# Optimization experiments

Measured on AMD Instinct MI355X. Metric: run time of the kernel, lower is better.

Reference implementation:

```python
import jax, jax.numpy as jnp
import numpy as np

N_NODES = 50000
IN_FEAT = 500
HIDDEN = 128
K = 2
N_CLASS = 16
E1 = 1000000
E2 = 1500000


def setup_inputs() -> dict:
    key = jax.random.key(0)
    ks = jax.random.split(key, 9)
    x = jax.random.normal(ks[0], (N_NODES, IN_FEAT), dtype=jnp.float32)
    a1_rows = jax.random.randint(ks[1], (E1,), 0, N_NODES, dtype=jnp.int32)
    a1_cols = jax.random.randint(ks[2], (E1,), 0, N_NODES, dtype=jnp.int32)
    a1_vals = jax.random.uniform(ks[3], (E1,), dtype=jnp.float32)
    a2_rows = jax.random.randint(ks[4], (E2,), 0, N_NODES, dtype=jnp.int32)
    a2_cols = jax.random.randint(ks[5], (E2,), 0, N_NODES, dtype=jnp.int32)
    a2_vals = jax.random.uniform(ks[6], (E2,), dtype=jnp.float32)
    w_embed = jax.random.normal(ks[7], (IN_FEAT, HIDDEN), dtype=jnp.float32) * 0.05
    w_classify = jax.random.normal(ks[8], ((2 ** (K + 1) - 1) * HIDDEN, N_CLASS), dtype=jnp.float32) * 0.05
    return {"x": x, "a1_rows": a1_rows, "a1_cols": a1_cols, "a1_vals": a1_vals,
            "a2_rows": a2_rows, "a2_cols": a2_cols, "a2_vals": a2_vals,
            "w_embed": w_embed, "w_classify": w_classify}


def _spmm(rows, cols, vals, r, n):
    # sparse [n,n] (COO) @ dense [n,d] -> gather sources, scale, scatter-add to rows
    return jax.ops.segment_sum(vals[:, None] * r[cols], rows, num_segments=n)


def reference(x, a1_rows, a1_cols, a1_vals, a2_rows, a2_cols, a2_vals, w_embed, w_classify):
    n = x.shape[0]
    rs = [jax.nn.relu(x @ w_embed)]  # [n, hidden]
    for _ in range(K):
        r_last = rs[-1]
        r1 = _spmm(a1_rows, a1_cols, a1_vals, r_last, n)
        r2 = _spmm(a2_rows, a2_cols, a2_vals, r_last, n)
        rs.append(jax.nn.relu(jnp.concatenate([r1, r2], axis=1)))
    r_final = jnp.concatenate(rs, axis=1)  # [n, (2^(k+1)-1)*hidden]
    # dropout is inactive in eval mode
    return jax.nn.softmax(r_final @ w_classify, axis=1)
```

## Files before the change

### kernel.cpp

```cpp
#include <hip/hip_runtime.h>
#include <hip/hip_fp16.h>

#define HID 128
#define INF 500
#define NCLS 16
#define PW  112
#define BKLG 8
#define BKW 256
#define NB1 128
#define NB2 192

typedef __attribute__((ext_vector_type(8))) short short8v;
typedef __attribute__((ext_vector_type(4))) float f32x4;
typedef __attribute__((ext_vector_type(4))) float f4v;

__device__ __forceinline__ void split_bf16(float v, unsigned short& h, unsigned short& l) {
  unsigned u = __float_as_uint(v);
  h = (unsigned short)(u >> 16);
  float hf = __uint_as_float(u & 0xFFFF0000u);
  l = (unsigned short)(__float_as_uint(v - hf) >> 16);
}

__device__ __forceinline__ void cvt8v(f4v c0, f4v c1, short8v& h8, short8v& l8) {
#pragma unroll
  for (int j = 0; j < 8; ++j) {
    float v = (j < 4) ? c0[j] : c1[j - 4];
    unsigned short h, l;
    split_bf16(v, h, l);
    h8[j] = (short)h;
    l8[j] = (short)l;
  }
}

__global__ __launch_bounds__(256) void prep_w(
    const float* __restrict__ we, const float* __restrict__ wc,
    unsigned short* __restrict__ wh, unsigned short* __restrict__ wl,
    unsigned short* __restrict__ ch, unsigned short* __restrict__ cl) {
  const int bid = blockIdx.x;
  if (bid < 256) {
    int idx = bid * 256 + threadIdx.x;
    int k = idx >> 7, nn = idx & 127;
    float v = (k < INF) ? we[k * HID + nn] : 0.f;
    unsigned short h, l;
    split_bf16(v, h, l);
    int kstep = k >> 5, ks = k & 31;
    int lane = (nn & 15) | ((ks >> 3) << 4);
    int j = ks & 7, nf = nn >> 4;
    size_t o = (((size_t)(kstep * 8 + nf)) * 64 + lane) * 8 + j;
    wh[o] = h;
    wl[o] = l;
  } else {
    int idx = (bid - 256) * 256 + threadIdx.x;
    if (idx >= HID * PW) return;
    int k = idx / PW, np = idx % PW;
    int o = np >> 4;
    int blk = (o == 0) ? 0 : ((o < 4) ? (2 * o - 1) : (2 * o - 6));
    float v = wc[(blk * HID + k) * NCLS + (np & 15)];
    unsigned short h, l;
    split_bf16(v, h, l);
    int kstep = k >> 5, ks = k & 31;
    int lane = (np & 15) | ((ks >> 3) << 4);
    int j = ks & 7, nf = np >> 4;
    size_t of = (((size_t)(kstep * 7 + nf)) * 64 + lane) * 8 + j;
    ch[of] = h;
    cl[of] = l;
  }
}

__global__ __launch_bounds__(128) void embed_mfma(
    const float* __restrict__ x, const unsigned short* __restrict__ wh,
    const unsigned short* __restrict__ wl, unsigned short* __restrict__ r0h,
    unsigned short* __restrict__ r0l, int n) {
  const int tid = threadIdx.x;
  const int wave = tid >> 6, lane = tid & 63;
  const int row0 = blockIdx.x * 64;
  const int rA = lane & 15, kg = lane >> 4;

  __shared__ float xs[64][68];

  f32x4 acc[2][8];
#pragma unroll
  for (int rf = 0; rf < 2; ++rf)
#pragma unroll
    for (int nf = 0; nf < 8; ++nf)
#pragma unroll
      for (int r = 0; r < 4; ++r) acc[rf][nf][r] = 0.f;

  f4v pf[8];
#define LOAD_TILE(kt)                                                         \
  {                                                                           \
    const int k0_ = (kt) * 64;                                                \
    _Pragma("unroll")                                                         \
    for (int q = 0; q < 8; ++q) {                                             \
      int i_ = tid + q * 128;                                                 \
      int r_ = i_ >> 4, pos_ = i_ & 15;                                       \
      int gr_ = min(row0 + r_, n - 1);                                        \
      int gk_ = k0_ + pos_ * 4;                                               \
      pf[q] = (gk_ + 4 <= INF)                                                \
                  ? __builtin_nontemporal_load(                               \
                        (const f4v*)&x[(size_t)gr_ * INF + gk_])              \
                  : (f4v)(0.f);                                               \
    }                                                                         \
  }

  LOAD_TILE(0);
  for (int kt = 0; kt < 8; ++kt) {
#pragma unroll
    for (int q = 0; q < 8; ++q) {
      int i = tid + q * 128;
      *(f4v*)&xs[i >> 4][(i & 15) * 4] = pf[q];
    }
    __syncthreads();
    if (kt < 7) LOAD_TILE(kt + 1);

#pragma unroll
    for (int kh2 = 0; kh2 < 2; ++kh2) {
      const int kb = kh2 * 32 + kg * 8;
      short8v ah[2], al[2];
#pragma unroll
      for (int rf = 0; rf < 2; ++rf) {
        const int rl = wave * 32 + rf * 16 + rA;
        f4v c0 = *(const f4v*)&xs[rl][kb];
        f4v c1 = *(const f4v*)&xs[rl][kb + 4];
        cvt8v(c0, c1, ah[rf], al[rf]);
      }
      const size_t bbase = ((size_t)((kt * 2 + kh2) * 8) * 64 + lane) * 8;
      short8v Bh[8], Bl[8];
#pragma unroll
      for (int nf = 0; nf < 8; ++nf) {
        Bh[nf] = *(const short8v*)&wh[bbase + (size_t)nf * 512];
        Bl[nf] = *(const short8v*)&wl[bbase + (size_t)nf * 512];
      }
#pragma unroll
      for (int nf = 0; nf < 8; ++nf)
#pragma unroll
        for (int rf = 0; rf < 2; ++rf) {
          acc[rf][nf] = __builtin_amdgcn_mfma_f32_16x16x32_bf16(ah[rf], Bh[nf], acc[rf][nf], 0, 0, 0);
          acc[rf][nf] = __builtin_amdgcn_mfma_f32_16x16x32_bf16(ah[rf], Bl[nf], acc[rf][nf], 0, 0, 0);
          acc[rf][nf] = __builtin_amdgcn_mfma_f32_16x16x32_bf16(al[rf], Bh[nf], acc[rf][nf], 0, 0, 0);
        }
    }
    __syncthreads();
  }
#undef LOAD_TILE

#pragma unroll
  for (int rf = 0; rf < 2; ++rf)
#pragma unroll
    for (int nf = 0; nf < 8; ++nf) {
      const int row = row0 + wave * 32 + rf * 16 + kg * 4;
      const int col = nf * 16 + rA;
#pragma unroll
      for (int r = 0; r < 4; ++r) {
        if (row + r < n) {
          float v = fmaxf(acc[rf][nf][r], 0.f);
          unsigned short h, l;
          split_bf16(v, h, l);
          r0h[(size_t)(row + r) * HID + col] = h;
          r0l[(size_t)(row + r) * HID + col] = l;
        }
      }
    }
}

__global__ __launch_bounds__(256) void proj_mfma(
    const unsigned short* __restrict__ r0h, const unsigned short* __restrict__ r0l,
    const unsigned short* __restrict__ ch, const unsigned short* __restrict__ cl,
    float* __restrict__ s0f, __half* __restrict__ Pa1, __half* __restrict__ Pa2, int n) {
  const int wave = threadIdx.x >> 6, lane = threadIdx.x & 63;
  const int row0 = blockIdx.x * 64 + wave * 16;
  const int rA = lane & 15, kg = lane >> 4;

  f32x4 acc[7];
#pragma unroll
  for (int nf = 0; nf < 7; ++nf)
#pragma unroll
    for (int r = 0; r < 4; ++r) acc[nf][r] = 0.f;

  const unsigned short* arh = &r0h[(size_t)min(row0 + rA, n - 1) * HID];
  const unsigned short* arl = &r0l[(size_t)min(row0 + rA, n - 1) * HID];

#pragma unroll
  for (int kstep = 0; kstep < 4; ++kstep) {
    const int kb = kstep * 32 + kg * 8;
    short8v ah = __builtin_nontemporal_load((const short8v*)&arh[kb]);
    short8v al = __builtin_nontemporal_load((const short8v*)&arl[kb]);

    const size_t bbase = ((size_t)kstep * 7 * 64 + lane) * 8;
    short8v Bh[7], Bl[7];
#pragma unroll
    for (int nf = 0; nf < 7; ++nf) {
      Bh[nf] = *(const short8v*)&ch[bbase + (size_t)nf * 512];
      Bl[nf] = *(const short8v*)&cl[bbase + (size_t)nf * 512];
    }
#pragma unroll
    for (int nf = 0; nf < 7; ++nf) {
      acc[nf] = __builtin_amdgcn_mfma_f32_16x16x32_bf16(ah, Bh[nf], acc[nf], 0, 0, 0);
      acc[nf] = __builtin_amdgcn_mfma_f32_16x16x32_bf16(ah, Bl[nf], acc[nf], 0, 0, 0);
      acc[nf] = __builtin_amdgcn_mfma_f32_16x16x32_bf16(al, Bh[nf], acc[nf], 0, 0, 0);
    }
  }

#pragma unroll
  for (int nf = 0; nf < 7; ++nf) {
    const int row = row0 + kg * 4;
#pragma unroll
    for (int r = 0; r < 4; ++r) {
      if (row + r < n) {
        float v = acc[nf][r];
        size_t ro = (size_t)(row + r) * 16 + rA;
        if (nf == 0) {
          s0f[ro] = v;
        } else if (nf < 4) {
          Pa1[ro * 4 + (nf - 1)] = __float2half(v);
          if (nf == 1) Pa1[ro * 4 + 3] = __float2half(0.f);
        } else {
          Pa2[ro * 4 + (nf - 4)] = __float2half(v);
          if (nf == 4) Pa2[ro * 4 + 3] = __float2half(0.f);
        }
      }
    }
  }
}

__global__ __launch_bounds__(256) void part_hist(
    const int* __restrict__ r1, int e1, const int* __restrict__ r2, int e2,
    int* __restrict__ g1, int* __restrict__ g2, int nbk) {
  const int m = blockIdx.y;
  const int NB = m ? NB2 : NB1;
  const int b = blockIdx.x;
  if (b >= NB) return;
  const int* rows = m ? r2 : r1;
  const int E = m ? e2 : e1;
  int* g = m ? g2 : g1;
  __shared__ int h[512];
  for (int i = threadIdx.x; i < nbk; i += 256) h[i] = 0;
  __syncthreads();
  const int ch = (E + NB - 1) / NB;
  const int lo = b * ch, hi = min(lo + ch, E);
  for (int i = lo + threadIdx.x; i < hi; i += 256)
    atomicAdd(&h[rows[i] >> BKLG], 1);
  __syncthreads();
  for (int k = threadIdx.x; k < nbk; k += 256) g[(size_t)k * NB + b] = h[k];
}

__global__ __launch_bounds__(256) void part_scan(
    int* __restrict__ g1, int m1, int* __restrict__ g2, int m2) {
  int* g = blockIdx.x ? g2 : g1;
  const int m = blockIdx.x ? m2 : m1;
  __shared__ int sh[256];
  const int t = threadIdx.x;
  const int chunk = (m + 255) >> 8;
  const int lo = t * chunk, hi = min(lo + chunk, m);
  int s = 0;
  for (int i = lo; i < hi; ++i) s += g[i];
  sh[t] = s;
  __syncthreads();
  for (int d = 1; d < 256; d <<= 1) {
    int v = (t >= d) ? sh[t - d] : 0;
    __syncthreads();
    sh[t] += v;
    __syncthreads();
  }
  int run = sh[t] - s;
  for (int i = lo; i < hi; ++i) { int v = g[i]; g[i] = run; run += v; }
}

__global__ __launch_bounds__(256) void part_scatter(
    const int* __restrict__ r1, const int* __restrict__ c1, const float* __restrict__ v1, int e1,
    const int* __restrict__ r2, const int* __restrict__ c2, const float* __restrict__ v2, int e2,
    const int* __restrict__ g1, const int* __restrict__ g2,
    int2* __restrict__ pack1, int2* __restrict__ pack2, int nbk) {
  const int m = blockIdx.y;
  const int NB = m ? NB2 : NB1;
  const int b = blockIdx.x;
  if (b >= NB) return;
  const int* rows = m ? r2 : r1;
  const int* cols = m ? c2 : c1;
  const float* vals = m ? v2 : v1;
  const int E = m ? e2 : e1;
  const int* g = m ? g2 : g1;
  int2* pack = m ? pack2 : pack1;
  __shared__ int lcur[512];
  for (int k = threadIdx.x; k < nbk; k += 256) lcur[k] = g[(size_t)k * NB + b];
  __syncthreads();
  const int ch = (E + NB - 1) / NB;
  const int lo = b * ch, hi = min(lo + ch, E);
  for (int i = lo + threadIdx.x; i < hi; i += 256) {
    int r = rows[i];
    int pos = atomicAdd(&lcur[r >> BKLG], 1);
    unsigned u = (unsigned)(vals[i] * 65536.0f);
    if (u > 65535u) u = 65535u;
    pack[pos] = make_int2(cols[i] | ((r & (BKW - 1)) << 16), (int)u);
  }
}

__global__ __launch_bounds__(256) void bucket_sort(
    const int2* __restrict__ pack1, const int* __restrict__ g1,
    unsigned* __restrict__ srt1, int* __restrict__ rp1, int e1,
    const int2* __restrict__ pack2, const int* __restrict__ g2,
    unsigned* __restrict__ srt2, int* __restrict__ rp2, int e2,
    int n, int nbk) {
  const int m = blockIdx.y;
  const int NB = m ? NB2 : NB1;
  const int2* pack = m ? pack2 : pack1;
  const int* g = m ? g2 : g1;
  unsigned* srt = m ? srt2 : srt1;
  int* rp = m ? rp2 : rp1;
  const int E = m ? e2 : e1;
  const int k = blockIdx.x;
  const int base = g[(size_t)k * NB];
  const int end = (k + 1 < nbk) ? g[(size_t)(k + 1) * NB] : E;
  __shared__ int lcnt[256], lws[256], lcur[256];
  const int t = threadIdx.x;
  lcnt[t] = 0;
  __syncthreads();
  for (int i = base + t; i < end; i += 256)
    atomicAdd(&lcnt[(pack[i].x >> 16) & (BKW - 1)], 1);
  __syncthreads();
  int s = lcnt[t];
  lws[t] = s;
  __syncthreads();
  for (int d = 1; d < 256; d <<= 1) {
    int v = (t >= d) ? lws[t - d] : 0;
    __syncthreads();
    lws[t] += v;
    __syncthreads();
  }
  int excl = base + lws[t] - s;
  lcur[t] = excl;
  int row = k * BKW + t;
  if (row < n) rp[row] = excl;
  if (k == nbk - 1 && t == 0) rp[n] = E;
  __syncthreads();
  for (int i = base + t; i < end; i += 256) {
    int2 e = pack[i];
    int pos = atomicAdd(&lcur[(e.x >> 16) & (BKW - 1)], 1);
    srt[pos] = (unsigned)(e.x & 0xFFFF) | ((unsigned)e.y << 16);
  }
}

__device__ __forceinline__ float dec_val(unsigned e) {
  return ((float)(e >> 16) + 0.5f) * (1.0f / 65536.0f);
}

__global__ __launch_bounds__(256) void spmm48_both(
    const unsigned* __restrict__ srt1, const int* __restrict__ rp1,
    const unsigned* __restrict__ srt2, const int* __restrict__ rp2,
    const __half* __restrict__ Pa1, const __half* __restrict__ Pa2,
    const float* __restrict__ s0f, float* __restrict__ wsum,
    __half* __restrict__ m3h, __half* __restrict__ m4h, int n) {
  const int row = blockIdx.x * 4 + (threadIdx.x >> 6);
  if (row >= n) return;
  const int lane = threadIdx.x & 63;
  const int c = lane & 15, g = lane >> 4;
  float a0 = 0.f, a1 = 0.f, a2 = 0.f, b0 = 0.f, b1 = 0.f, b2 = 0.f;
  {
    const int j0 = rp1[row], j1 = rp1[row + 1];
    if (j1 > j0) {
      const int nit = (j1 - j0 + 15) >> 4;
      int j = j0 + g;
      for (int it = 0; it < nit; ++it, j += 16) {
        int jj0 = min(j, j1 - 1), jj1 = min(j + 4, j1 - 1);
        int jj2 = min(j + 8, j1 - 1), jj3 = min(j + 12, j1 - 1);
        unsigned e0 = __builtin_nontemporal_load(&srt1[jj0]);
        unsigned e1 = __builtin_nontemporal_load(&srt1[jj1]);
        unsigned e2 = __builtin_nontemporal_load(&srt1[jj2]);
        unsigned e3 = __builtin_nontemporal_load(&srt1[jj3]);
        float2 r0 = *(const float2*)(Pa1 + ((size_t)(e0 & 0xFFFF) * 16 + c) * 4);
        float2 r1 = *(const float2*)(Pa1 + ((size_t)(e1 & 0xFFFF) * 16 + c) * 4);
        float2 r2 = *(const float2*)(Pa1 + ((size_t)(e2 & 0xFFFF) * 16 + c) * 4);
        float2 r3 = *(const float2*)(Pa1 + ((size_t)(e3 & 0xFFFF) * 16 + c) * 4);
        float v0 = (j < j1) ? dec_val(e0) : 0.f;
        float v1 = (j + 4 < j1) ? dec_val(e1) : 0.f;
        float v2 = (j + 8 < j1) ? dec_val(e2) : 0.f;
        float v3 = (j + 12 < j1) ? dec_val(e3) : 0.f;
        float2 f00 = __half22float2(*(__half2*)&r0.x), f01 = __half22float2(*(__half2*)&r0.y);
        float2 f10 = __half22float2(*(__half2*)&r1.x), f11 = __half22float2(*(__half2*)&r1.y);
        float2 f20 = __half22float2(*(__half2*)&r2.x), f21 = __half22float2(*(__half2*)&r2.y);
        float2 f30 = __half22float2(*(__half2*)&r3.x), f31 = __half22float2(*(__half2*)&r3.y);
        a0 += v0 * f00.x + v1 * f10.x + v2 * f20.x + v3 * f30.x;
        a1 += v0 * f00.y + v1 * f10.y + v2 * f20.y + v3 * f30.y;
        a2 += v0 * f01.x + v1 * f11.x + v2 * f21.x + v3 * f31.x;
      }
    }
  }
  {
    const int j0 = rp2[row], j1 = rp2[row + 1];
    if (j1 > j0) {
      const int nit = (j1 - j0 + 15) >> 4;
      int j = j0 + g;
      for (int it = 0; it < nit; ++it, j += 16) {
        int jj0 = min(j, j1 - 1), jj1 = min(j + 4, j1 - 1);
        int jj2 = min(j + 8, j1 - 1), jj3 = min(j + 12, j1 - 1);
        unsigned e0 = __builtin_nontemporal_load(&srt2[jj0]);
        unsigned e1 = __builtin_nontemporal_load(&srt2[jj1]);
        unsigned e2 = __builtin_nontemporal_load(&srt2[jj2]);
        unsigned e3 = __builtin_nontemporal_load(&srt2[jj3]);
        float2 r0 = *(const float2*)(Pa2 + ((size_t)(e0 & 0xFFFF) * 16 + c) * 4);
        float2 r1 = *(const float2*)(Pa2 + ((size_t)(e1 & 0xFFFF) * 16 + c) * 4);
        float2 r2 = *(const float2*)(Pa2 + ((size_t)(e2 & 0xFFFF) * 16 + c) * 4);
        float2 r3 = *(const float2*)(Pa2 + ((size_t)(e3 & 0xFFFF) * 16 + c) * 4);
        float v0 = (j < j1) ? dec_val(e0) : 0.f;
        float v1 = (j + 4 < j1) ? dec_val(e1) : 0.f;
        float v2 = (j + 8 < j1) ? dec_val(e2) : 0.f;
        float v3 = (j + 12 < j1) ? dec_val(e3) : 0.f;
        float2 f00 = __half22float2(*(__half2*)&r0.x), f01 = __half22float2(*(__half2*)&r0.y);
        float2 f10 = __half22float2(*(__half2*)&r1.x), f11 = __half22float2(*(__half2*)&r1.y);
        float2 f20 = __half22float2(*(__half2*)&r2.x), f21 = __half22float2(*(__half2*)&r2.y);
        float2 f30 = __half22float2(*(__half2*)&r3.x), f31 = __half22float2(*(__half2*)&r3.y);
        b0 += v0 * f00.x + v1 * f10.x + v2 * f20.x + v3 * f30.x;
        b1 += v0 * f00.y + v1 * f10.y + v2 * f20.y + v3 * f30.y;
        b2 += v0 * f01.x + v1 * f11.x + v2 * f21.x + v3 * f31.x;
      }
    }
  }
  a0 += __shfl_xor(a0, 16); a0 += __shfl_xor(a0, 32);
  a1 += __shfl_xor(a1, 16); a1 += __shfl_xor(a1, 32);
  a2 += __shfl_xor(a2, 16); a2 += __shfl_xor(a2, 32);
  b0 += __shfl_xor(b0, 16); b0 += __shfl_xor(b0, 32);
  b1 += __shfl_xor(b1, 16); b1 += __shfl_xor(b1, 32);
  b2 += __shfl_xor(b2, 16); b2 += __shfl_xor(b2, 32);
  if (g == 0) {
    size_t ro = (size_t)row * 16 + c;
    wsum[ro] = s0f[ro] + a0 + b0;
    m3h[ro] = __float2half(a1 + b1);
    m4h[ro] = __float2half(a2 + b2);
  }
}

__global__ __launch_bounds__(256) void final_spmm_softmax(
    const unsigned* __restrict__ srt1, const int* __restrict__ rp1,
    const unsigned* __restrict__ srt2, const int* __restrict__ rp2,
    const float* __restrict__ wsum, const __half* __restrict__ m3h,
    const __half* __restrict__ m4h, float* __restrict__ out, int n) {
  const int row = blockIdx.x * 4 + (threadIdx.x >> 6);
  if (row >= n) return;
  const int lane = threadIdx.x & 63;
  const int c = lane & 15, g = lane >> 4;
  float accA = 0.f, accB = 0.f;
  {
    const int j0 = rp1[row], j1 = rp1[row + 1];
    if (j1 > j0) {
      const int nit = (j1 - j0 + 15) >> 4;
      int j = j0 + g;
      for (int it = 0; it < nit; ++it, j += 16) {
        int jj0 = min(j, j1 - 1), jj1 = min(j + 4, j1 - 1);
        int jj2 = min(j + 8, j1 - 1), jj3 = min(j + 12, j1 - 1);
        unsigned e0 = __builtin_nontemporal_load(&srt1[jj0]);
        unsigned e1 = __builtin_nontemporal_load(&srt1[jj1]);
        unsigned e2 = __builtin_nontemporal_load(&srt1[jj2]);
        unsigned e3 = __builtin_nontemporal_load(&srt1[jj3]);
        float g0 = __half2float(m3h[(size_t)(e0 & 0xFFFF) * 16 + c]);
        float g1 = __half2float(m3h[(size_t)(e1 & 0xFFFF) * 16 + c]);
        float g2 = __half2float(m3h[(size_t)(e2 & 0xFFFF) * 16 + c]);
        float g3 = __half2float(m3h[(size_t)(e3 & 0xFFFF) * 16 + c]);
        float v0 = (j < j1) ? dec_val(e0) : 0.f;
        float v1 = (j + 4 < j1) ? dec_val(e1) : 0.f;
        float v2 = (j + 8 < j1) ? dec_val(e2) : 0.f;
        float v3 = (j + 12 < j1) ? dec_val(e3) : 0.f;
        accA += v0 * g0 + v1 * g1 + v2 * g2 + v3 * g3;
      }
    }
  }
  {
    const int j0 = rp2[row], j1 = rp2[row + 1];
    if (j1 > j0) {
      const int nit = (j1 - j0 + 15) >> 4;
      int j = j0 + g;
      for (int it = 0; it < nit; ++it, j += 16) {
        int jj0 = min(j, j1 - 1), jj1 = min(j + 4, j1 - 1);
        int jj2 = min(j + 8, j1 - 1), jj3 = min(j + 12, j1 - 1);
        unsigned e0 = __builtin_nontemporal_load(&srt2[jj0]);
        unsigned e1 = __builtin_nontemporal_load(&srt2[jj1]);
        unsigned e2 = __builtin_nontemporal_load(&srt2[jj2]);
        unsigned e3 = __builtin_nontemporal_load(&srt2[jj3]);
        float g0 = __half2float(m4h[(size_t)(e0 & 0xFFFF) * 16 + c]);
        float g1 = __half2float(m4h[(size_t)(e1 & 0xFFFF) * 16 + c]);
        float g2 = __half2float(m4h[(size_t)(e2 & 0xFFFF) * 16 + c]);
        float g3 = __half2float(m4h[(size_t)(e3 & 0xFFFF) * 16 + c]);
        float v0 = (j < j1) ? dec_val(e0) : 0.f;
        float v1 = (j + 4 < j1) ? dec_val(e1) : 0.f;
        float v2 = (j + 8 < j1) ? dec_val(e2) : 0.f;
        float v3 = (j + 12 < j1) ? dec_val(e3) : 0.f;
        accB += v0 * g0 + v1 * g1 + v2 * g2 + v3 * g3;
      }
    }
  }
  accA += __shfl_xor(accA, 16); accA += __shfl_xor(accA, 32);
  accB += __shfl_xor(accB, 16); accB += __shfl_xor(accB, 32);
  float logit = wsum[(size_t)row * 16 + c] + accA + accB;
  float m = logit;
#pragma unroll
  for (int off = 1; off < 16; off <<= 1) m = fmaxf(m, __shfl_xor(m, off));
  float e = __expf(logit - m);
  float s = e;
#pragma unroll
  for (int off = 1; off < 16; off <<= 1) s += __shfl_xor(s, off);
  float p = e / s;
  if (lane < 16) out[(size_t)row * NCLS + lane] = p;
}

extern "C" void kernel_launch(void* const* d_in, const int* in_sizes, int n_in,
                              void* d_out, int out_size, void* d_ws, size_t ws_size,
                              hipStream_t stream) {
  const float* x   = (const float*)d_in[0];
  const int*   a1r = (const int*)d_in[1];
  const int*   a1c = (const int*)d_in[2];
  const float* a1v = (const float*)d_in[3];
  const int*   a2r = (const int*)d_in[4];
  const int*   a2c = (const int*)d_in[5];
  const float* a2v = (const float*)d_in[6];
  const float* we  = (const float*)d_in[7];
  const float* wc  = (const float*)d_in[8];
  const int n  = in_sizes[0] / INF;
  const int e1 = in_sizes[1];
  const int e2 = in_sizes[4];
  const int nbk = (n + BKW - 1) >> BKLG;

  char* w = (char*)d_ws;
  size_t off = 0;
  unsigned short* r0h = (unsigned short*)(w + off); off += (size_t)n * HID * 2;
  unsigned short* r0l = (unsigned short*)(w + off); off += (size_t)n * HID * 2;
  float* s0f  = (float*)(w + off); off += (size_t)n * 16 * 4;
  __half* Pa1 = (__half*)(w + off); off += (size_t)n * 64 * 2;
  __half* Pa2 = (__half*)(w + off); off += (size_t)n * 64 * 2;
  float* wsum = (float*)(w + off); off += (size_t)n * 16 * 4;
  __half* m3h = (__half*)(w + off); off += (size_t)n * 16 * 2;
  __half* m4h = (__half*)(w + off); off += (size_t)n * 16 * 2;
  int2* pack1 = (int2*)(w + off);  off += (size_t)e1 * 8;
  int2* pack2 = (int2*)(w + off);  off += (size_t)e2 * 8;
  unsigned* srt1 = (unsigned*)(w + off); off += (size_t)e1 * 4;
  unsigned* srt2 = (unsigned*)(w + off); off += (size_t)e2 * 4;
  unsigned short* wefh = (unsigned short*)(w + off); off += (size_t)512 * HID * 2;
  unsigned short* wefl = (unsigned short*)(w + off); off += (size_t)512 * HID * 2;
  unsigned short* wcfh = (unsigned short*)(w + off); off += (size_t)HID * PW * 2;
  unsigned short* wcfl = (unsigned short*)(w + off); off += (size_t)HID * PW * 2;
  int* g1 = (int*)(w + off); off += (size_t)512 * NB1 * 4;
  int* g2 = (int*)(w + off); off += (size_t)512 * NB2 * 4;
  int* rp1 = (int*)(w + off); off += (size_t)(n + 1) * 4;
  int* rp2 = (int*)(w + off); off += (size_t)(n + 1) * 4;

  prep_w<<<312, 256, 0, stream>>>(we, wc, wefh, wefl, wcfh, wcfl);
  embed_mfma<<<(n + 63) / 64, 128, 0, stream>>>(x, wefh, wefl, r0h, r0l, n);
  proj_mfma<<<(n + 63) / 64, 256, 0, stream>>>(r0h, r0l, wcfh, wcfl, s0f, Pa1, Pa2, n);

  part_hist<<<dim3(NB2, 2), 256, 0, stream>>>(a1r, e1, a2r, e2, g1, g2, nbk);
  part_scan<<<2, 256, 0, stream>>>(g1, nbk * NB1, g2, nbk * NB2);
  part_scatter<<<dim3(NB2, 2), 256, 0, stream>>>(
      a1r, a1c, a1v, e1, a2r, a2c, a2v, e2, g1, g2, pack1, pack2, nbk);
  bucket_sort<<<dim3(nbk, 2), 256, 0, stream>>>(
      pack1, g1, srt1, rp1, e1, pack2, g2, srt2, rp2, e2, n, nbk);

  spmm48_both<<<(n + 3) / 4, 256, 0, stream>>>(
      srt1, rp1, srt2, rp2, Pa1, Pa2, s0f, wsum, m3h, m4h, n);
  final_spmm_softmax<<<(n + 3) / 4, 256, 0, stream>>>(
      srt1, rp1, srt2, rp2, wsum, m3h, m4h, (float*)d_out, n);
}
```

Before: 284.8 us.

## Replace single-block offset scan with per-bucket totals and parallel per-bucket scans

The two-block serial scan over the bucket-by-block histogram matrix is replaced by three steps. The histogram kernel now also accumulates per-bucket totals with global atomics. A small kernel scans those totals, and a grid of one block per bucket and matrix then scans each bucket's block counts in parallel. This removes the long serial per-thread loops of the old two-block scan. In exchange it adds an extra launch, a memset and global atomics.

Result: faster. 242.5 us (-14.8%).

```diff
diff --git a/kernel.cpp b/kernel.cpp
--- a/kernel.cpp
+++ b/kernel.cpp
@@ -225,7 +225,8 @@
 
 __global__ __launch_bounds__(256) void part_hist(
     const int* __restrict__ r1, int e1, const int* __restrict__ r2, int e2,
-    int* __restrict__ g1, int* __restrict__ g2, int nbk) {
+    int* __restrict__ g1, int* __restrict__ g2,
+    int* __restrict__ bt1, int* __restrict__ bt2, int nbk) {
   const int m = blockIdx.y;
   const int NB = m ? NB2 : NB1;
   const int b = blockIdx.x;
@@ -233,6 +234,7 @@
   const int* rows = m ? r2 : r1;
   const int E = m ? e2 : e1;
   int* g = m ? g2 : g1;
+  int* bt = m ? bt2 : bt1;
   __shared__ int h[512];
   for (int i = threadIdx.x; i < nbk; i += 256) h[i] = 0;
   __syncthreads();
@@ -241,29 +243,51 @@
   for (int i = lo + threadIdx.x; i < hi; i += 256)
     atomicAdd(&h[rows[i] >> BKLG], 1);
   __syncthreads();
-  for (int k = threadIdx.x; k < nbk; k += 256) g[(size_t)k * NB + b] = h[k];
-}
-
-__global__ __launch_bounds__(256) void part_scan(
-    int* __restrict__ g1, int m1, int* __restrict__ g2, int m2) {
-  int* g = blockIdx.x ? g2 : g1;
-  const int m = blockIdx.x ? m2 : m1;
+  for (int k = threadIdx.x; k < nbk; k += 256) {
+    g[(size_t)k * NB + b] = h[k];
+    if (h[k]) atomicAdd(&bt[k], h[k]);
+  }
+}
+
+__global__ __launch_bounds__(256) void scan_bt(
+    const int* __restrict__ bt1, int* __restrict__ ebt1,
+    const int* __restrict__ bt2, int* __restrict__ ebt2, int nbk) {
+  const int* bt = blockIdx.x ? bt2 : bt1;
+  int* ebt = blockIdx.x ? ebt2 : ebt1;
   __shared__ int sh[256];
   const int t = threadIdx.x;
-  const int chunk = (m + 255) >> 8;
-  const int lo = t * chunk, hi = min(lo + chunk, m);
-  int s = 0;
-  for (int i = lo; i < hi; ++i) s += g[i];
-  sh[t] = s;
+  int v = (t < nbk) ? bt[t] : 0;
+  sh[t] = v;
   __syncthreads();
   for (int d = 1; d < 256; d <<= 1) {
-    int v = (t >= d) ? sh[t - d] : 0;
-    __syncthreads();
-    sh[t] += v;
-    __syncthreads();
-  }
-  int run = sh[t] - s;
-  for (int i = lo; i < hi; ++i) { int v = g[i]; g[i] = run; run += v; }
+    int u = (t >= d) ? sh[t - d] : 0;
+    __syncthreads();
+    sh[t] += u;
+    __syncthreads();
+  }
+  if (t < nbk) ebt[t] = sh[t] - v;
+}
+
+__global__ __launch_bounds__(256) void offs_scan(
+    int* __restrict__ g1, const int* __restrict__ ebt1,
+    int* __restrict__ g2, const int* __restrict__ ebt2, int nbk) {
+  const int m = blockIdx.y;
+  const int NB = m ? NB2 : NB1;
+  int* g = m ? g2 : g1;
+  const int* ebt = m ? ebt2 : ebt1;
+  const int k = blockIdx.x;
+  __shared__ int sh[256];
+  const int t = threadIdx.x;
+  int v = (t < NB) ? g[(size_t)k * NB + t] : 0;
+  sh[t] = v;
+  __syncthreads();
+  for (int d = 1; d < 256; d <<= 1) {
+    int u = (t >= d) ? sh[t - d] : 0;
+    __syncthreads();
+    sh[t] += u;
+    __syncthreads();
+  }
+  if (t < NB) g[(size_t)k * NB + t] = ebt[k] + sh[t] - v;
 }
 
 __global__ __launch_bounds__(256) void part_scatter(
@@ -540,13 +564,20 @@
   int* g2 = (int*)(w + off); off += (size_t)512 * NB2 * 4;
   int* rp1 = (int*)(w + off); off += (size_t)(n + 1) * 4;
   int* rp2 = (int*)(w + off); off += (size_t)(n + 1) * 4;
+  int* bt1  = (int*)(w + off); off += (size_t)512 * 4;
+  int* bt2  = (int*)(w + off); off += (size_t)512 * 4;
+  int* ebt1 = (int*)(w + off); off += (size_t)512 * 4;
+  int* ebt2 = (int*)(w + off); off += (size_t)512 * 4;
+
+  hipMemsetAsync(bt1, 0, (size_t)2 * 512 * sizeof(int), stream);
 
   prep_w<<<312, 256, 0, stream>>>(we, wc, wefh, wefl, wcfh, wcfl);
   embed_mfma<<<(n + 63) / 64, 128, 0, stream>>>(x, wefh, wefl, r0h, r0l, n);
   proj_mfma<<<(n + 63) / 64, 256, 0, stream>>>(r0h, r0l, wcfh, wcfl, s0f, Pa1, Pa2, n);
 
-  part_hist<<<dim3(NB2, 2), 256, 0, stream>>>(a1r, e1, a2r, e2, g1, g2, nbk);
-  part_scan<<<2, 256, 0, stream>>>(g1, nbk * NB1, g2, nbk * NB2);
+  part_hist<<<dim3(NB2, 2), 256, 0, stream>>>(a1r, e1, a2r, e2, g1, g2, bt1, bt2, nbk);
+  scan_bt<<<2, 256, 0, stream>>>(bt1, ebt1, bt2, ebt2, nbk);
+  offs_scan<<<dim3(nbk, 2), 256, 0, stream>>>(g1, ebt1, g2, ebt2, nbk);
   part_scatter<<<dim3(NB2, 2), 256, 0, stream>>>(
       a1r, a1c, a1v, e1, a2r, a2c, a2v, e2, g1, g2, pack1, pack2, nbk);
   bucket_sort<<<dim3(nbk, 2), 256, 0, stream>>>(
```
